# Optimization experiments

Hardware: AMD Instinct MI355X
Metric: run time of the kernel (lower is better)

The kernel has to match this reference:

```python
import jax, jax.numpy as jnp
import numpy as np

IN_C = 256
HID_C = 256
HEADS = 8
SCALE = 1.0 / np.sqrt(HID_C / HEADS).astype(np.float32)


def setup_inputs() -> dict:
    key = jax.random.key(0)
    k_v, k_q, k_k, k_w, k_o, k_b = jax.random.split(key, 6)
    B, S = 4, 2048
    lim_in = 1.0 / np.sqrt(IN_C)
    lim_out = 1.0 / np.sqrt(IN_C * HEADS)
    v = jax.random.normal(k_v, (B, S, IN_C), dtype=jnp.float32)
    WQ = jax.random.uniform(k_q, (IN_C, IN_C * HEADS), jnp.float32, -lim_in, lim_in)
    WK = jax.random.uniform(k_k, (IN_C, IN_C * HEADS), jnp.float32, -lim_in, lim_in)
    WV = jax.random.uniform(k_w, (IN_C, IN_C * HEADS), jnp.float32, -lim_in, lim_in)
    Wout = jax.random.uniform(k_o, (IN_C * HEADS, HID_C), jnp.float32, -lim_out, lim_out)
    bout = jax.random.uniform(k_b, (HID_C,), jnp.float32, -lim_out, lim_out)
    return {"v": v, "WQ": WQ, "WK": WK, "WV": WV, "Wout": Wout, "bout": bout}


def reference(v, WQ, WK, WV, Wout, bout):
    B, S, C = v.shape  # C == IN_C
    H = HEADS
    # projections, reshape to [b, s, h, c] (per-head dim == in_channels)
    q = (v @ WQ).reshape(B, S, H, C)
    k = (v @ WK).reshape(B, S, H, C)
    val = (v @ WV).reshape(B, S, H, C)
    # scores [b, s1, s2, h]; softmax over s2 (axis=-2 of this layout)
    scores = jnp.einsum('bshc,bthc->bsth', q, k) * SCALE
    A = jax.nn.softmax(scores, axis=2)
    u = jnp.einsum('bsth,bthc->bshc', A, val).reshape(B, S, H * C)
    return u @ Wout + bout
```

## Files before the change

### kernel.cpp

```cpp
#include <hip/hip_runtime.h>
#include <hip/hip_bf16.h>

typedef __bf16 bf16x8 __attribute__((ext_vector_type(8)));
typedef float f32x4 __attribute__((ext_vector_type(4)));
typedef unsigned short ushort8 __attribute__((ext_vector_type(8)));

#define DEVINL static __device__ __forceinline__

DEVINL unsigned f2bf(float f){
  unsigned u = __float_as_uint(f);
  return (u + 0x7fffu + ((u >> 16) & 1u)) >> 16;
}

DEVINL f32x4 MFMA(bf16x8 a, bf16x8 b, f32x4 c){
  return __builtin_amdgcn_mfma_f32_16x16x32_bf16(a, b, c, 0, 0, 0);
}

typedef const __attribute__((address_space(1))) unsigned int* gas_t;
typedef __attribute__((address_space(3))) unsigned int* las_t;
DEVINL void gload_lds16(const void* g, void* l){
  __builtin_amdgcn_global_load_lds((gas_t)g, (las_t)l, 16, 0, 0);
}

__global__ void k_cvt(const float* __restrict__ s, unsigned short* __restrict__ d, int n){
  int i = (blockIdx.x * blockDim.x + threadIdx.x) * 4;
  if (i >= n) return;
  float4 v = *(const float4*)(s + i);
  ushort4 o;
  o.x = (unsigned short)f2bf(v.x); o.y = (unsigned short)f2bf(v.y);
  o.z = (unsigned short)f2bf(v.z); o.w = (unsigned short)f2bf(v.w);
  *(ushort4*)(d + i) = o;
}

__global__ void k_tr(const float* __restrict__ s, unsigned short* __restrict__ d, int R, int C){
  __shared__ float t[32][33];
  int c0 = blockIdx.x * 32, r0 = blockIdx.y * 32;
  int tx = threadIdx.x, ty = threadIdx.y;
  #pragma unroll
  for (int k2 = 0; k2 < 4; k2++) t[ty + 8*k2][tx] = s[(r0 + ty + 8*k2) * C + c0 + tx];
  __syncthreads();
  #pragma unroll
  for (int k2 = 0; k2 < 4; k2++) d[(c0 + ty + 8*k2) * R + r0 + tx] = (unsigned short)f2bf(t[tx][ty + 8*k2]);
}

__global__ __launch_bounds__(256, 2) void k_qkv(const unsigned short* __restrict__ vb,
    const unsigned short* __restrict__ wT,
    unsigned short* __restrict__ qo, unsigned short* __restrict__ ko, unsigned short* __restrict__ vTo){
  __shared__ unsigned short As[128 * 72];
  __shared__ unsigned short Bs[128 * 72];
  int tid = threadIdx.x;
  int lane = tid & 63, wid = tid >> 6;
  int lr = lane & 15, lg = lane >> 4;
  int wm = (wid >> 1) * 64, wn = (wid & 1) * 64;
  int bn = blockIdx.x, bm = blockIdx.y, z = blockIdx.z;

  const unsigned short* Ag = vb + (bm * 128) * 256;
  const unsigned short* Bg = wT + z * (2048 * 256) + (bn * 128) * 256;

  f32x4 acc[4][4] = {};
  for (int kt = 0; kt < 4; kt++){
    ushort8 ra[4], rb[4];
    #pragma unroll
    for (int p = 0; p < 4; p++){
      int idx = p * 256 + tid; int row = idx >> 3, ch = idx & 7;
      ra[p] = *(const ushort8*)(Ag + row * 256 + kt * 64 + ch * 8);
      rb[p] = *(const ushort8*)(Bg + row * 256 + kt * 64 + ch * 8);
    }
    __syncthreads();
    #pragma unroll
    for (int p = 0; p < 4; p++){
      int idx = p * 256 + tid; int row = idx >> 3, ch = idx & 7;
      *(ushort8*)(As + row * 72 + ch * 8) = ra[p];
      *(ushort8*)(Bs + row * 72 + ch * 8) = rb[p];
    }
    __syncthreads();
    #pragma unroll
    for (int kf = 0; kf < 2; kf++){
      bf16x8 af[4], bfr[4];
      #pragma unroll
      for (int mf = 0; mf < 4; mf++) af[mf]  = *(const bf16x8*)(As + (wm + mf*16 + lr) * 72 + kf*32 + lg*8);
      #pragma unroll
      for (int nf = 0; nf < 4; nf++) bfr[nf] = *(const bf16x8*)(Bs + (wn + nf*16 + lr) * 72 + kf*32 + lg*8);
      #pragma unroll
      for (int mf = 0; mf < 4; mf++)
        #pragma unroll
        for (int nf = 0; nf < 4; nf++)
          acc[mf][nf] = MFMA(af[mf], bfr[nf], acc[mf][nf]);
    }
  }
  if (z < 2){
    unsigned short* dst = z ? ko : qo;
    #pragma unroll
    for (int mf = 0; mf < 4; mf++)
      #pragma unroll
      for (int nf = 0; nf < 4; nf++){
        int mg = bm*128 + wm + mf*16 + lg*4;
        int ng = bn*128 + wn + nf*16 + lr;
        #pragma unroll
        for (int r2 = 0; r2 < 4; r2++) dst[(mg + r2) * 2048 + ng] = (unsigned short)f2bf(acc[mf][nf][r2]);
      }
  } else {
    #pragma unroll
    for (int mf = 0; mf < 4; mf++)
      #pragma unroll
      for (int nf = 0; nf < 4; nf++){
        int mg = bm*128 + wm + mf*16 + lg*4;
        int ng = bn*128 + wn + nf*16 + lr;
        int bb = mg >> 11, s = mg & 2047, hh = ng >> 8, cc = ng & 255;
        uint2 w;
        w.x = f2bf(acc[mf][nf][0]) | (f2bf(acc[mf][nf][1]) << 16);
        w.y = f2bf(acc[mf][nf][2]) | (f2bf(acc[mf][nf][3]) << 16);
        *(uint2*)(vTo + (size_t)((bb*8 + hh) * 256 + cc) * 2048 + s) = w;
      }
  }
}

__global__ __launch_bounds__(256, 2) void k_attn(const unsigned short* __restrict__ q,
    const unsigned short* __restrict__ kk, const unsigned short* __restrict__ vT,
    unsigned short* __restrict__ u){
  __shared__ unsigned short Ks[2][8192];
  __shared__ unsigned short Vs[2][8192];
  __shared__ unsigned short Ps[4][1024];
  int tid = threadIdx.x;
  int lane = tid & 63, wid = tid >> 6;
  int lr = lane & 15, lg = lane >> 4;
  int g = (blockIdx.x & 7) * 64 + (blockIdx.x >> 3);
  int bh = g >> 4, qt = g & 15;
  int b = bh >> 3, h = bh & 7;
  int q0 = qt * 128;

  const char* kgB = (const char*)(kk + (size_t)b * 2048 * 2048 + h * 256);
  const char* vgB = (const char*)(vT + (size_t)(b * 8 + h) * 256 * 2048);
  const unsigned short* qg = q + (size_t)(b * 2048 + q0 + wid * 32) * 2048 + h * 256;

  const char* sp[8];
  bool isK = wid < 2;
  long stepB = isK ? 131072 : 64;
  #pragma unroll
  for (int j = 0; j < 8; j++){
    if (isK){
      int c = wid * 512 + j * 64 + lane;
      int row = c >> 5, slot = c & 31;
      sp[j] = kgB + (size_t)row * 4096 + ((slot ^ (row & 7)) * 16);
    } else {
      int c2 = (wid - 2) * 512 + j * 64 + lane;
      int crow = c2 >> 2, slot = c2 & 3;
      sp[j] = vgB + (size_t)crow * 4096 + ((slot ^ (crow & 3)) * 16);
    }
  }
  int wbase = (wid & 1) * 8192;
  auto stage = [&](int buf){
    char* db = (char*)(isK ? &Ks[buf][0] : &Vs[buf][0]) + wbase;
    #pragma unroll
    for (int j = 0; j < 8; j++){
      gload_lds16(sp[j], db + j * 1024);
      sp[j] += stepB;
    }
  };

  stage(0);

  bf16x8 qreg[2][8];
  #pragma unroll
  for (int qf = 0; qf < 2; qf++)
    #pragma unroll
    for (int kf = 0; kf < 8; kf++)
      qreg[qf][kf] = *(const bf16x8*)(qg + (size_t)(qf * 16 + lr) * 2048 + kf * 32 + lg * 8);

  f32x4 acc[2][16] = {};
  float lpart[2] = {0.f, 0.f};
  const float SC2   = 0.25503510f;
  const float SHIFT = -11.5415603f;

  for (int t0 = 0; t0 < 64; t0++){
    int cur = t0 & 1;
    asm volatile("s_waitcnt vmcnt(0)" ::: "memory");
    __builtin_amdgcn_s_barrier();
    if (t0 + 1 < 64) stage(cur ^ 1);
    const unsigned short* Ksb = Ks[cur];
    const unsigned short* Vsb = Vs[cur];
    unsigned short* Psw = Ps[wid];

    f32x4 pt[2][2] = {};
    __builtin_amdgcn_s_setprio(1);
    #pragma unroll
    for (int kf = 0; kf < 8; kf++){
      #pragma unroll
      for (int tf = 0; tf < 2; tf++){
        int row = tf * 16 + lr;
        bf16x8 ka = *(const bf16x8*)(Ksb + row * 256 + (((kf * 4 + lg) ^ (row & 7)) * 8));
        pt[tf][0] = MFMA(ka, qreg[0][kf], pt[tf][0]);
        pt[tf][1] = MFMA(ka, qreg[1][kf], pt[tf][1]);
      }
    }
    __builtin_amdgcn_s_setprio(0);
    #pragma unroll
    for (int qf = 0; qf < 2; qf++){
      float s0 = 0.f, s1 = 0.f;
      #pragma unroll
      for (int tf = 0; tf < 2; tf++)
        #pragma unroll
        for (int r2 = 0; r2 < 4; r2++){
          float e = __builtin_amdgcn_exp2f(fmaf(pt[tf][qf][r2], SC2, SHIFT));
          pt[tf][qf][r2] = e;
          if (r2 & 1) s1 += e; else s0 += e;
        }
      lpart[qf] += s0 + s1;
    }
    #pragma unroll
    for (int qf = 0; qf < 2; qf++){
      int qrow = qf * 16 + lr;
      #pragma unroll
      for (int tf = 0; tf < 2; tf++){
        uint2 w;
        w.x = f2bf(pt[tf][qf][0]) | (f2bf(pt[tf][qf][1]) << 16);
        w.y = f2bf(pt[tf][qf][2]) | (f2bf(pt[tf][qf][3]) << 16);
        *(uint2*)(Psw + qrow * 32 + (((tf * 2 + (lg >> 1)) ^ (qrow & 3)) * 8) + (lg & 1) * 4) = w;
      }
    }
    bf16x8 pa0 = *(const bf16x8*)(Psw + lr * 32 + ((lg ^ (lr & 3)) * 8));
    bf16x8 pa1 = *(const bf16x8*)(Psw + (16 + lr) * 32 + ((lg ^ (lr & 3)) * 8));
    __builtin_amdgcn_s_setprio(1);
    #pragma unroll
    for (int nf = 0; nf < 16; nf++){
      int crow = nf * 16 + lr;
      bf16x8 vf = *(const bf16x8*)(Vsb + crow * 32 + ((lg ^ (crow & 3)) * 8));
      acc[0][nf] = MFMA(pa0, vf, acc[0][nf]);
      acc[1][nf] = MFMA(pa1, vf, acc[1][nf]);
    }
    __builtin_amdgcn_s_setprio(0);
  }
  #pragma unroll
  for (int qf = 0; qf < 2; qf++){
    lpart[qf] += __shfl_xor(lpart[qf], 16);
    lpart[qf] += __shfl_xor(lpart[qf], 32);
  }
  #pragma unroll
  for (int mf = 0; mf < 2; mf++){
    float inv = 1.f / lpart[mf];
    float i4[4];
    #pragma unroll
    for (int r2 = 0; r2 < 4; r2++) i4[r2] = __shfl(inv, lg * 4 + r2);
    #pragma unroll
    for (int nf = 0; nf < 16; nf++)
      #pragma unroll
      for (int r2 = 0; r2 < 4; r2++){
        int s = q0 + wid * 32 + mf * 16 + lg * 4 + r2;
        int c = nf * 16 + lr;
        u[(size_t)(b * 2048 + s) * 2048 + h * 256 + c] = (unsigned short)f2bf(acc[mf][nf][r2] * i4[r2]);
      }
  }
}

__global__ __launch_bounds__(256, 2) void k_out(const unsigned short* __restrict__ u,
    const unsigned short* __restrict__ woT, const float* __restrict__ bout, float* __restrict__ out){
  __shared__ unsigned short As[64 * 72];
  __shared__ unsigned short Bs[64 * 72];
  int tid = threadIdx.x;
  int lane = tid & 63, wid = tid >> 6;
  int lr = lane & 15, lg = lane >> 4;
  int wm = (wid >> 1) * 32, wn = (wid & 1) * 32;
  int bn = blockIdx.x, bm = blockIdx.y;
  const unsigned short* Ag = u + (size_t)(bm * 64) * 2048;
  const unsigned short* Bg = woT + (size_t)(bn * 64) * 2048;
  f32x4 acc[2][2] = {};
  for (int kt = 0; kt < 32; kt++){
    ushort8 ra[2], rb[2];
    #pragma unroll
    for (int p = 0; p < 2; p++){
      int idx = p * 256 + tid; int row = idx >> 3, ch = idx & 7;
      ra[p] = *(const ushort8*)(Ag + (size_t)row * 2048 + kt*64 + ch*8);
      rb[p] = *(const ushort8*)(Bg + (size_t)row * 2048 + kt*64 + ch*8);
    }
    __syncthreads();
    #pragma unroll
    for (int p = 0; p < 2; p++){
      int idx = p * 256 + tid; int row = idx >> 3, ch = idx & 7;
      *(ushort8*)(As + row * 72 + ch * 8) = ra[p];
      *(ushort8*)(Bs + row * 72 + ch * 8) = rb[p];
    }
    __syncthreads();
    #pragma unroll
    for (int kf = 0; kf < 2; kf++){
      bf16x8 a0 = *(const bf16x8*)(As + (wm + lr) * 72      + kf*32 + lg*8);
      bf16x8 a1 = *(const bf16x8*)(As + (wm + 16 + lr) * 72 + kf*32 + lg*8);
      bf16x8 b0 = *(const bf16x8*)(Bs + (wn + lr) * 72      + kf*32 + lg*8);
      bf16x8 b1 = *(const bf16x8*)(Bs + (wn + 16 + lr) * 72 + kf*32 + lg*8);
      acc[0][0] = MFMA(a0, b0, acc[0][0]); acc[0][1] = MFMA(a0, b1, acc[0][1]);
      acc[1][0] = MFMA(a1, b0, acc[1][0]); acc[1][1] = MFMA(a1, b1, acc[1][1]);
    }
  }
  #pragma unroll
  for (int mf = 0; mf < 2; mf++)
    #pragma unroll
    for (int nf = 0; nf < 2; nf++){
      int mg = bm*64 + wm + mf*16 + lg*4;
      int ng = bn*64 + wn + nf*16 + lr;
      #pragma unroll
      for (int r2 = 0; r2 < 4; r2++) out[(size_t)(mg + r2) * 256 + ng] = acc[mf][nf][r2] + bout[ng];
    }
}

extern "C" void kernel_launch(void* const* d_in, const int* in_sizes, int n_in,
                              void* d_out, int out_size, void* d_ws, size_t ws_size,
                              hipStream_t stream){
  const float* v    = (const float*)d_in[0];
  const float* WQ   = (const float*)d_in[1];
  const float* WK   = (const float*)d_in[2];
  const float* WV   = (const float*)d_in[3];
  const float* Wout = (const float*)d_in[4];
  const float* bout = (const float*)d_in[5];
  char* ws = (char*)d_ws;
  unsigned short* vb  = (unsigned short*)(ws);
  unsigned short* wT  = (unsigned short*)(ws + (4u  << 20));
  unsigned short* woT = (unsigned short*)(ws + (7u  << 20));
  unsigned short* qb  = (unsigned short*)(ws + (8u  << 20));
  unsigned short* kb  = (unsigned short*)(ws + (40u << 20));
  unsigned short* vTb = (unsigned short*)(ws + (72u << 20));
  unsigned short* ub  = (unsigned short*)(ws + (104u << 20));
  float* out = (float*)d_out;

  k_cvt<<<2048, 256, 0, stream>>>(v, vb, 2097152);
  k_tr<<<dim3(64, 8), dim3(32, 8), 0, stream>>>(WQ,   wT,           256, 2048);
  k_tr<<<dim3(64, 8), dim3(32, 8), 0, stream>>>(WK,   wT + 524288,  256, 2048);
  k_tr<<<dim3(64, 8), dim3(32, 8), 0, stream>>>(WV,   wT + 1048576, 256, 2048);
  k_tr<<<dim3(8, 64), dim3(32, 8), 0, stream>>>(Wout, woT,         2048, 256);
  k_qkv<<<dim3(16, 64, 3), 256, 0, stream>>>(vb, wT, qb, kb, vTb);
  k_attn<<<512, 256, 0, stream>>>(qb, kb, vTb, ub);
  k_out<<<dim3(4, 128), 256, 0, stream>>>(ub, woT, bout, out);
}
```

Measured before the change: 224.6 us.

## Use 8 waves per attention block with 16 query rows each, and merge transpose launches

The attention kernel now runs 512 threads (8 waves) per block. Each wave owns 16 query rows instead of 32, which halves the accumulator and Q register footprint. Staging of the K/V tiles is spread over 4 waves each instead of 2. The aim is more resident waves to hide LDS and MFMA latency, but each K/V fragment read from LDS is now reused by only one MFMA instead of two, so LDS read traffic per FLOP doubles. Separately, the four weight-transpose launches are merged into one kernel to cut launch overhead.

Result: slower. 286.1 us (+27.4%).

```diff
diff --git a/kernel.cpp b/kernel.cpp
--- a/kernel.cpp
+++ b/kernel.cpp
@@ -32,9 +32,21 @@
   *(ushort4*)(d + i) = o;
 }
 
-__global__ void k_tr(const float* __restrict__ s, unsigned short* __restrict__ d, int R, int C){
+__global__ void k_tr4(const float* __restrict__ WQ, const float* __restrict__ WK,
+                      const float* __restrict__ WV, const float* __restrict__ Wout,
+                      unsigned short* __restrict__ wT, unsigned short* __restrict__ woT){
   __shared__ float t[32][33];
-  int c0 = blockIdx.x * 32, r0 = blockIdx.y * 32;
+  int id = blockIdx.x;
+  const float* s; unsigned short* d; int R, C, tile;
+  if (id < 1536){
+    int z = id >> 9; tile = id & 511;
+    s = (z == 0) ? WQ : ((z == 1) ? WK : WV);
+    d = wT + z * 524288; R = 256; C = 2048;
+  } else {
+    tile = id - 1536; s = Wout; d = woT; R = 2048; C = 256;
+  }
+  int tilesX = C >> 5;
+  int c0 = (tile % tilesX) * 32, r0 = (tile / tilesX) * 32;
   int tx = threadIdx.x, ty = threadIdx.y;
   #pragma unroll
   for (int k2 = 0; k2 < 4; k2++) t[ty + 8*k2][tx] = s[(r0 + ty + 8*k2) * C + c0 + tx];
@@ -115,12 +127,12 @@
   }
 }
 
-__global__ __launch_bounds__(256, 2) void k_attn(const unsigned short* __restrict__ q,
+__global__ __launch_bounds__(512, 4) void k_attn(const unsigned short* __restrict__ q,
     const unsigned short* __restrict__ kk, const unsigned short* __restrict__ vT,
     unsigned short* __restrict__ u){
   __shared__ unsigned short Ks[2][8192];
   __shared__ unsigned short Vs[2][8192];
-  __shared__ unsigned short Ps[4][1024];
+  __shared__ unsigned short Ps[8][512];
   int tid = threadIdx.x;
   int lane = tid & 63, wid = tid >> 6;
   int lr = lane & 15, lg = lane >> 4;
@@ -131,28 +143,28 @@
 
   const char* kgB = (const char*)(kk + (size_t)b * 2048 * 2048 + h * 256);
   const char* vgB = (const char*)(vT + (size_t)(b * 8 + h) * 256 * 2048);
-  const unsigned short* qg = q + (size_t)(b * 2048 + q0 + wid * 32) * 2048 + h * 256;
-
-  const char* sp[8];
-  bool isK = wid < 2;
+  const unsigned short* qg = q + (size_t)(b * 2048 + q0 + wid * 16) * 2048 + h * 256;
+
+  const char* sp[4];
+  bool isK = wid < 4;
   long stepB = isK ? 131072 : 64;
   #pragma unroll
-  for (int j = 0; j < 8; j++){
+  for (int j = 0; j < 4; j++){
     if (isK){
-      int c = wid * 512 + j * 64 + lane;
+      int c = wid * 256 + j * 64 + lane;
       int row = c >> 5, slot = c & 31;
       sp[j] = kgB + (size_t)row * 4096 + ((slot ^ (row & 7)) * 16);
     } else {
-      int c2 = (wid - 2) * 512 + j * 64 + lane;
+      int c2 = (wid - 4) * 256 + j * 64 + lane;
       int crow = c2 >> 2, slot = c2 & 3;
       sp[j] = vgB + (size_t)crow * 4096 + ((slot ^ (crow & 3)) * 16);
     }
   }
-  int wbase = (wid & 1) * 8192;
+  int wbase = (isK ? wid : (wid - 4)) * 4096;
   auto stage = [&](int buf){
     char* db = (char*)(isK ? &Ks[buf][0] : &Vs[buf][0]) + wbase;
     #pragma unroll
-    for (int j = 0; j < 8; j++){
+    for (int j = 0; j < 4; j++){
       gload_lds16(sp[j], db + j * 1024);
       sp[j] += stepB;
     }
@@ -160,15 +172,13 @@
 
   stage(0);
 
-  bf16x8 qreg[2][8];
-  #pragma unroll
-  for (int qf = 0; qf < 2; qf++)
-    #pragma unroll
-    for (int kf = 0; kf < 8; kf++)
-      qreg[qf][kf] = *(const bf16x8*)(qg + (size_t)(qf * 16 + lr) * 2048 + kf * 32 + lg * 8);
-
-  f32x4 acc[2][16] = {};
-  float lpart[2] = {0.f, 0.f};
+  bf16x8 qreg[8];
+  #pragma unroll
+  for (int kf = 0; kf < 8; kf++)
+    qreg[kf] = *(const bf16x8*)(qg + (size_t)lr * 2048 + kf * 32 + lg * 8);
+
+  f32x4 acc[16] = {};
+  float lpart = 0.f;
   const float SC2   = 0.25503510f;
   const float SHIFT = -11.5415603f;
 
@@ -181,7 +191,7 @@
     const unsigned short* Vsb = Vs[cur];
     unsigned short* Psw = Ps[wid];
 
-    f32x4 pt[2][2] = {};
+    f32x4 pt[2] = {};
     __builtin_amdgcn_s_setprio(1);
     #pragma unroll
     for (int kf = 0; kf < 8; kf++){
@@ -189,55 +199,46 @@
       for (int tf = 0; tf < 2; tf++){
         int row = tf * 16 + lr;
         bf16x8 ka = *(const bf16x8*)(Ksb + row * 256 + (((kf * 4 + lg) ^ (row & 7)) * 8));
-        pt[tf][0] = MFMA(ka, qreg[0][kf], pt[tf][0]);
-        pt[tf][1] = MFMA(ka, qreg[1][kf], pt[tf][1]);
+        pt[tf] = MFMA(ka, qreg[kf], pt[tf]);
       }
     }
     __builtin_amdgcn_s_setprio(0);
-    #pragma unroll
-    for (int qf = 0; qf < 2; qf++){
+    {
       float s0 = 0.f, s1 = 0.f;
       #pragma unroll
       for (int tf = 0; tf < 2; tf++)
         #pragma unroll
         for (int r2 = 0; r2 < 4; r2++){
-          float e = __builtin_amdgcn_exp2f(fmaf(pt[tf][qf][r2], SC2, SHIFT));
-          pt[tf][qf][r2] = e;
+          float e = __builtin_amdgcn_exp2f(fmaf(pt[tf][r2], SC2, SHIFT));
+          pt[tf][r2] = e;
           if (r2 & 1) s1 += e; else s0 += e;
         }
-      lpart[qf] += s0 + s1;
-    }
-    #pragma unroll
-    for (int qf = 0; qf < 2; qf++){
-      int qrow = qf * 16 + lr;
+      lpart += s0 + s1;
+    }
+    {
+      int qrow = lr;
       #pragma unroll
       for (int tf = 0; tf < 2; tf++){
         uint2 w;
-        w.x = f2bf(pt[tf][qf][0]) | (f2bf(pt[tf][qf][1]) << 16);
-        w.y = f2bf(pt[tf][qf][2]) | (f2bf(pt[tf][qf][3]) << 16);
+        w.x = f2bf(pt[tf][0]) | (f2bf(pt[tf][1]) << 16);
+        w.y = f2bf(pt[tf][2]) | (f2bf(pt[tf][3]) << 16);
         *(uint2*)(Psw + qrow * 32 + (((tf * 2 + (lg >> 1)) ^ (qrow & 3)) * 8) + (lg & 1) * 4) = w;
       }
     }
-    bf16x8 pa0 = *(const bf16x8*)(Psw + lr * 32 + ((lg ^ (lr & 3)) * 8));
-    bf16x8 pa1 = *(const bf16x8*)(Psw + (16 + lr) * 32 + ((lg ^ (lr & 3)) * 8));
+    bf16x8 pa = *(const bf16x8*)(Psw + lr * 32 + ((lg ^ (lr & 3)) * 8));
     __builtin_amdgcn_s_setprio(1);
     #pragma unroll
     for (int nf = 0; nf < 16; nf++){
       int crow = nf * 16 + lr;
       bf16x8 vf = *(const bf16x8*)(Vsb + crow * 32 + ((lg ^ (crow & 3)) * 8));
-      acc[0][nf] = MFMA(pa0, vf, acc[0][nf]);
-      acc[1][nf] = MFMA(pa1, vf, acc[1][nf]);
+      acc[nf] = MFMA(pa, vf, acc[nf]);
     }
     __builtin_amdgcn_s_setprio(0);
   }
-  #pragma unroll
-  for (int qf = 0; qf < 2; qf++){
-    lpart[qf] += __shfl_xor(lpart[qf], 16);
-    lpart[qf] += __shfl_xor(lpart[qf], 32);
-  }
-  #pragma unroll
-  for (int mf = 0; mf < 2; mf++){
-    float inv = 1.f / lpart[mf];
+  lpart += __shfl_xor(lpart, 16);
+  lpart += __shfl_xor(lpart, 32);
+  {
+    float inv = 1.f / lpart;
     float i4[4];
     #pragma unroll
     for (int r2 = 0; r2 < 4; r2++) i4[r2] = __shfl(inv, lg * 4 + r2);
@@ -245,9 +246,9 @@
     for (int nf = 0; nf < 16; nf++)
       #pragma unroll
       for (int r2 = 0; r2 < 4; r2++){
-        int s = q0 + wid * 32 + mf * 16 + lg * 4 + r2;
+        int s = q0 + wid * 16 + lg * 4 + r2;
         int c = nf * 16 + lr;
-        u[(size_t)(b * 2048 + s) * 2048 + h * 256 + c] = (unsigned short)f2bf(acc[mf][nf][r2] * i4[r2]);
+        u[(size_t)(b * 2048 + s) * 2048 + h * 256 + c] = (unsigned short)f2bf(acc[nf][r2] * i4[r2]);
       }
   }
 }
@@ -321,11 +322,8 @@
   float* out = (float*)d_out;
 
   k_cvt<<<2048, 256, 0, stream>>>(v, vb, 2097152);
-  k_tr<<<dim3(64, 8), dim3(32, 8), 0, stream>>>(WQ,   wT,           256, 2048);
-  k_tr<<<dim3(64, 8), dim3(32, 8), 0, stream>>>(WK,   wT + 524288,  256, 2048);
-  k_tr<<<dim3(64, 8), dim3(32, 8), 0, stream>>>(WV,   wT + 1048576, 256, 2048);
-  k_tr<<<dim3(8, 64), dim3(32, 8), 0, stream>>>(Wout, woT,         2048, 256);
+  k_tr4<<<2048, dim3(32, 8), 0, stream>>>(WQ, WK, WV, Wout, wT, woT);
   k_qkv<<<dim3(16, 64, 3), 256, 0, stream>>>(vb, wT, qb, kb, vTb);
-  k_attn<<<512, 256, 0, stream>>>(qb, kb, vTb, ub);
+  k_attn<<<512, 512, 0, stream>>>(qb, kb, vTb, ub);
   k_out<<<dim3(4, 128), 256, 0, stream>>>(ub, woT, bout, out);
 }
```

## Keep attention P in registers via permlane swaps and merge weight transposes

Applied to the files above, without the earlier changes.

In the attention kernel, the P tile no longer makes a round trip through LDS. The exp results are packed with v_cvt_pk_bf16_f32 and rearranged across lanes with v_permlane32/16 swaps into the MFMA A-operand layout. This needs a new swizzled staging layout for the transposed V tile, and the K-fragment loads are reordered into paired even/odd k-chunks. The four weight-transpose launches are merged into one k_tr4 launch to cut launch overhead. The lane-permutation and swizzle mapping must be exactly right or results will be wrong.

After: 207.2 us. -7.7%, faster.

```diff
diff --git a/kernel.cpp b/kernel.cpp
--- a/kernel.cpp
+++ b/kernel.cpp
@@ -21,6 +21,12 @@
 DEVINL void gload_lds16(const void* g, void* l){
   __builtin_amdgcn_global_load_lds((gas_t)g, (las_t)l, 16, 0, 0);
 }
+
+DEVINL unsigned cvtpk(float lo, float hi){
+  unsigned r; asm("v_cvt_pk_bf16_f32 %0, %1, %2" : "=v"(r) : "v"(lo), "v"(hi)); return r;
+}
+DEVINL void sw32(unsigned &a, unsigned &b){ asm("v_permlane32_swap_b32 %0, %1" : "+v"(a), "+v"(b)); }
+DEVINL void sw16(unsigned &a, unsigned &b){ asm("v_permlane16_swap_b32 %0, %1" : "+v"(a), "+v"(b)); }
 
 __global__ void k_cvt(const float* __restrict__ s, unsigned short* __restrict__ d, int n){
   int i = (blockIdx.x * blockDim.x + threadIdx.x) * 4;
@@ -32,9 +38,21 @@
   *(ushort4*)(d + i) = o;
 }
 
-__global__ void k_tr(const float* __restrict__ s, unsigned short* __restrict__ d, int R, int C){
+__global__ void k_tr4(const float* __restrict__ WQ, const float* __restrict__ WK,
+                      const float* __restrict__ WV, const float* __restrict__ Wout,
+                      unsigned short* __restrict__ wT, unsigned short* __restrict__ woT){
   __shared__ float t[32][33];
-  int c0 = blockIdx.x * 32, r0 = blockIdx.y * 32;
+  int id = blockIdx.x;
+  const float* s; unsigned short* d; int R, C, tile;
+  if (id < 1536){
+    int z = id >> 9; tile = id & 511;
+    s = (z == 0) ? WQ : ((z == 1) ? WK : WV);
+    d = wT + z * 524288; R = 256; C = 2048;
+  } else {
+    tile = id - 1536; s = Wout; d = woT; R = 2048; C = 256;
+  }
+  int tilesX = C >> 5;
+  int c0 = (tile % tilesX) * 32, r0 = (tile / tilesX) * 32;
   int tx = threadIdx.x, ty = threadIdx.y;
   #pragma unroll
   for (int k2 = 0; k2 < 4; k2++) t[ty + 8*k2][tx] = s[(r0 + ty + 8*k2) * C + c0 + tx];
@@ -120,7 +138,6 @@
     unsigned short* __restrict__ u){
   __shared__ unsigned short Ks[2][8192];
   __shared__ unsigned short Vs[2][8192];
-  __shared__ unsigned short Ps[4][1024];
   int tid = threadIdx.x;
   int lane = tid & 63, wid = tid >> 6;
   int lr = lane & 15, lg = lane >> 4;
@@ -144,8 +161,9 @@
       sp[j] = kgB + (size_t)row * 4096 + ((slot ^ (row & 7)) * 16);
     } else {
       int c2 = (wid - 2) * 512 + j * 64 + lane;
-      int crow = c2 >> 2, slot = c2 & 3;
-      sp[j] = vgB + (size_t)crow * 4096 + ((slot ^ (crow & 3)) * 16);
+      int blk = c2 >> 5, ts = (c2 >> 3) & 3, low3 = c2 & 7;
+      int crow = blk * 8 + (low3 ^ (ts * 2));
+      sp[j] = vgB + (size_t)crow * 4096 + ts * 16;
     }
   }
   int wbase = (wid & 1) * 8192;
@@ -171,29 +189,40 @@
   float lpart[2] = {0.f, 0.f};
   const float SC2   = 0.25503510f;
   const float SHIFT = -11.5415603f;
+
+  int xA = (lg ^ (lr & 7)) * 16;
+  int vbase = (lr >> 3) * 512 + lg * 128 + (((lr & 7) ^ (lg * 2)) * 16);
 
   for (int t0 = 0; t0 < 64; t0++){
     int cur = t0 & 1;
     asm volatile("s_waitcnt vmcnt(0)" ::: "memory");
     __builtin_amdgcn_s_barrier();
     if (t0 + 1 < 64) stage(cur ^ 1);
-    const unsigned short* Ksb = Ks[cur];
-    const unsigned short* Vsb = Vs[cur];
-    unsigned short* Psw = Ps[wid];
+    const char* Kc = (const char*)Ks[cur];
+    const char* Vc = (const char*)Vs[cur];
 
     f32x4 pt[2][2] = {};
+    const char* ka0 = Kc + lr * 512 + xA;
+    const char* ka1 = Kc + lr * 512 + (xA ^ 64);
     __builtin_amdgcn_s_setprio(1);
     #pragma unroll
-    for (int kf = 0; kf < 8; kf++){
-      #pragma unroll
-      for (int tf = 0; tf < 2; tf++){
-        int row = tf * 16 + lr;
-        bf16x8 ka = *(const bf16x8*)(Ksb + row * 256 + (((kf * 4 + lg) ^ (row & 7)) * 8));
-        pt[tf][0] = MFMA(ka, qreg[0][kf], pt[tf][0]);
-        pt[tf][1] = MFMA(ka, qreg[1][kf], pt[tf][1]);
-      }
+    for (int kf2 = 0; kf2 < 4; kf2++){
+      bf16x8 kE0 = *(const bf16x8*)(ka0 + kf2 * 128);
+      bf16x8 kO0 = *(const bf16x8*)(ka1 + kf2 * 128);
+      bf16x8 kE1 = *(const bf16x8*)(ka0 + 8192 + kf2 * 128);
+      bf16x8 kO1 = *(const bf16x8*)(ka1 + 8192 + kf2 * 128);
+      pt[0][0] = MFMA(kE0, qreg[0][2*kf2],   pt[0][0]);
+      pt[0][1] = MFMA(kE0, qreg[1][2*kf2],   pt[0][1]);
+      pt[1][0] = MFMA(kE1, qreg[0][2*kf2],   pt[1][0]);
+      pt[1][1] = MFMA(kE1, qreg[1][2*kf2],   pt[1][1]);
+      pt[0][0] = MFMA(kO0, qreg[0][2*kf2+1], pt[0][0]);
+      pt[0][1] = MFMA(kO0, qreg[1][2*kf2+1], pt[0][1]);
+      pt[1][0] = MFMA(kO1, qreg[0][2*kf2+1], pt[1][0]);
+      pt[1][1] = MFMA(kO1, qreg[1][2*kf2+1], pt[1][1]);
     }
     __builtin_amdgcn_s_setprio(0);
+
+    bf16x8 pa[2];
     #pragma unroll
     for (int qf = 0; qf < 2; qf++){
       float s0 = 0.f, s1 = 0.f;
@@ -206,27 +235,23 @@
           if (r2 & 1) s1 += e; else s0 += e;
         }
       lpart[qf] += s0 + s1;
-    }
-    #pragma unroll
-    for (int qf = 0; qf < 2; qf++){
-      int qrow = qf * 16 + lr;
-      #pragma unroll
-      for (int tf = 0; tf < 2; tf++){
-        uint2 w;
-        w.x = f2bf(pt[tf][qf][0]) | (f2bf(pt[tf][qf][1]) << 16);
-        w.y = f2bf(pt[tf][qf][2]) | (f2bf(pt[tf][qf][3]) << 16);
-        *(uint2*)(Psw + qrow * 32 + (((tf * 2 + (lg >> 1)) ^ (qrow & 3)) * 8) + (lg & 1) * 4) = w;
-      }
-    }
-    bf16x8 pa0 = *(const bf16x8*)(Psw + lr * 32 + ((lg ^ (lr & 3)) * 8));
-    bf16x8 pa1 = *(const bf16x8*)(Psw + (16 + lr) * 32 + ((lg ^ (lr & 3)) * 8));
+      unsigned A = cvtpk(pt[0][qf][0], pt[0][qf][1]);
+      unsigned B = cvtpk(pt[0][qf][2], pt[0][qf][3]);
+      unsigned C = cvtpk(pt[1][qf][0], pt[1][qf][1]);
+      unsigned D = cvtpk(pt[1][qf][2], pt[1][qf][3]);
+      sw32(A, C); sw32(B, D);
+      sw16(A, C); sw16(B, D);
+      union { unsigned w[4]; bf16x8 v; } cv;
+      cv.w[0] = A; cv.w[1] = B; cv.w[2] = C; cv.w[3] = D;
+      pa[qf] = cv.v;
+    }
+
     __builtin_amdgcn_s_setprio(1);
     #pragma unroll
     for (int nf = 0; nf < 16; nf++){
-      int crow = nf * 16 + lr;
-      bf16x8 vf = *(const bf16x8*)(Vsb + crow * 32 + ((lg ^ (crow & 3)) * 8));
-      acc[0][nf] = MFMA(pa0, vf, acc[0][nf]);
-      acc[1][nf] = MFMA(pa1, vf, acc[1][nf]);
+      bf16x8 vf = *(const bf16x8*)(Vc + nf * 1024 + vbase);
+      acc[0][nf] = MFMA(pa[0], vf, acc[0][nf]);
+      acc[1][nf] = MFMA(pa[1], vf, acc[1][nf]);
     }
     __builtin_amdgcn_s_setprio(0);
   }
@@ -321,10 +346,7 @@
   float* out = (float*)d_out;
 
   k_cvt<<<2048, 256, 0, stream>>>(v, vb, 2097152);
-  k_tr<<<dim3(64, 8), dim3(32, 8), 0, stream>>>(WQ,   wT,           256, 2048);
-  k_tr<<<dim3(64, 8), dim3(32, 8), 0, stream>>>(WK,   wT + 524288,  256, 2048);
-  k_tr<<<dim3(64, 8), dim3(32, 8), 0, stream>>>(WV,   wT + 1048576, 256, 2048);
-  k_tr<<<dim3(8, 64), dim3(32, 8), 0, stream>>>(Wout, woT,         2048, 256);
+  k_tr4<<<2048, dim3(32, 8), 0, stream>>>(WQ, WK, WV, Wout, wT, woT);
   k_qkv<<<dim3(16, 64, 3), 256, 0, stream>>>(vb, wT, qb, kb, vTb);
   k_attn<<<512, 256, 0, stream>>>(qb, kb, vTb, ub);
   k_out<<<dim3(4, 128), 256, 0, stream>>>(ub, woT, bout, out);
```
